# Kernel optimization log

Measured on AMD Instinct MI355X. Metric: run time of the kernel, lower is better.

## Reference

```python
import jax, jax.numpy as jnp
import numpy as np

K = 10
ALPHA = 0.1
N_NODES = 100000
N_EDGES = 3200000
FEATURES = 512
HIDDEN = 256
CLASSES = 64


def setup_inputs() -> dict:
    key = jax.random.key(0)
    k1, k2, k3, k4 = jax.random.split(key, 4)
    x = jax.random.normal(k1, (N_NODES, FEATURES), dtype=jnp.float32)
    edge_index = jax.random.randint(k2, (2, N_EDGES), 0, N_NODES, dtype=jnp.int64)
    W1 = jax.random.normal(k3, (FEATURES, HIDDEN), dtype=jnp.float32) * (1.0 / np.sqrt(FEATURES))
    b1 = jnp.zeros((HIDDEN,), dtype=jnp.float32)
    W2 = jax.random.normal(k4, (HIDDEN, CLASSES), dtype=jnp.float32) * (1.0 / np.sqrt(HIDDEN))
    b2 = jnp.zeros((CLASSES,), dtype=jnp.float32)
    return {"x": x, "edge_index": edge_index, "W1": W1, "b1": b1, "W2": W2, "b2": b2}


def _gcn_norm(edge_index, n_nodes):
    # Add self-loops (APPNP / GCN normalization: D^-1/2 (A+I) D^-1/2)
    loops = jnp.arange(n_nodes, dtype=edge_index.dtype)
    row = jnp.concatenate([edge_index[0], loops])
    col = jnp.concatenate([edge_index[1], loops])
    ones = jnp.ones(row.shape[0], dtype=jnp.float32)
    deg = jax.ops.segment_sum(ones, col, num_segments=n_nodes)
    dinv = jnp.where(deg > 0, jax.lax.rsqrt(deg), 0.0)
    norm = dinv[row] * dinv[col]
    return row, col, norm


def reference(x, edge_index, W1, b1, W2, b2):
    n = x.shape[0]
    h = jax.nn.relu(x @ W1 + b1)          # [N, hidden]
    h = h @ W2 + b2                        # [N, classes]
    row, col, norm = _gcn_norm(edge_index, n)

    def step(out, _):
        msg = out[col] * norm[:, None]     # gather + scale over edges
        agg = jax.ops.segment_sum(msg, row, num_segments=n)
        return (1.0 - ALPHA) * agg + ALPHA * h, None

    out, _ = jax.lax.scan(step, h, None, length=K)
    return jax.nn.log_softmax(out, axis=1)
```

## Files before the change

kernel.cpp:

```cpp
#include <hip/hip_runtime.h>
#include <hip/hip_bf16.h>
#include <math.h>

#define N_NODES 100000
#define N_EDGES 3200000
#define FEAT 512
#define HID 256
#define CLS 64
#define K_ITER 10
#define NBUCK 196
#define BSH 9

typedef _Float16 half8 __attribute__((ext_vector_type(8)));
typedef float f32x4 __attribute__((ext_vector_type(4)));

__device__ __forceinline__ int edge_at(const void* e, int is64, long long idx) {
    return is64 ? (int)((const long long*)e)[idx] : ((const int*)e)[idx];
}

__global__ void k_detect(const unsigned* __restrict__ e, int* __restrict__ flag) {
    __shared__ unsigned s[256];
    unsigned v = 0;
    for (int i = threadIdx.x; i < 4096; i += 256) v |= e[2 * i + 1];
    s[threadIdx.x] = v;
    __syncthreads();
    for (int off = 128; off; off >>= 1) {
        if (threadIdx.x < off) s[threadIdx.x] |= s[threadIdx.x + off];
        __syncthreads();
    }
    if (threadIdx.x == 0) flag[0] = (s[0] == 0) ? 1 : 0;
}

__global__ void k_init(int* __restrict__ bcntR, int* __restrict__ bcntC) {
    for (int i = threadIdx.x; i < NBUCK; i += 256) { bcntR[i] = 0; bcntC[i] = 0; }
}

#define CHB 4096
__global__ __launch_bounds__(256) void k_bhist(const void* __restrict__ e,
                                               const int* __restrict__ flag,
                                               int* __restrict__ bcntR,
                                               int* __restrict__ bcntC) {
    __shared__ int lhR[NBUCK], lhC[NBUCK];
    for (int i = threadIdx.x; i < NBUCK; i += 256) { lhR[i] = 0; lhC[i] = 0; }
    __syncthreads();
    int is64 = flag[0];
    long long base = (long long)blockIdx.x * CHB;
    for (int j = threadIdx.x; j < CHB; j += 256) {
        long long i = base + j;
        if (i < N_EDGES) {
            int r = edge_at(e, is64, i);
            int c = edge_at(e, is64, (long long)N_EDGES + i);
            atomicAdd(&lhR[r >> BSH], 1);
            atomicAdd(&lhC[c >> BSH], 1);
        }
    }
    __syncthreads();
    for (int i = threadIdx.x; i < NBUCK; i += 256) {
        if (lhR[i]) atomicAdd(&bcntR[i], lhR[i]);
        if (lhC[i]) atomicAdd(&bcntC[i], lhC[i]);
    }
}

__global__ void k_bscan(const int* __restrict__ bcntR, const int* __restrict__ bcntC,
                        int* __restrict__ bbaseR, int* __restrict__ gcurR,
                        int* __restrict__ bbaseC, int* __restrict__ gcurC,
                        int* __restrict__ cbase, int* __restrict__ offs) {
    if (threadIdx.x == 0) {
        int accE = 0, accC = 0, accCv = 0;
        for (int b = 0; b < NBUCK; b++) {
            bbaseR[b] = accE;
            gcurR[b] = accE;
            bbaseC[b] = accCv;
            gcurC[b] = accCv;
            cbase[b] = accC;
            int nb0 = b << BSH;
            int nn = (N_NODES - nb0 < 512) ? (N_NODES - nb0) : 512;
            accE += bcntR[b];
            accCv += bcntC[b];
            accC += bcntR[b] + nn;
        }
        bbaseR[NBUCK] = accE;
        bbaseC[NBUCK] = accCv;
        cbase[NBUCK] = accC;
        offs[N_NODES] = accC;
    }
}

#define CH 4096
__global__ __launch_bounds__(256) void k_binA(const void* __restrict__ e,
                                              const int* __restrict__ flag,
                                              int* __restrict__ gcurR,
                                              int* __restrict__ gcurC,
                                              unsigned long long* __restrict__ pairs,
                                              int* __restrict__ cvals) {
    __shared__ int lhR[NBUCK], gbR[NBUCK], lcR[NBUCK];
    __shared__ int lhC[NBUCK], gbC[NBUCK], lcC[NBUCK];
    for (int i = threadIdx.x; i < NBUCK; i += 256) { lhR[i] = 0; lhC[i] = 0; }
    __syncthreads();
    int is64 = flag[0];
    long long base = (long long)blockIdx.x * CH;
    for (int j = threadIdx.x; j < CH; j += 256) {
        long long i = base + j;
        if (i < N_EDGES) {
            int r = edge_at(e, is64, i);
            int c = edge_at(e, is64, (long long)N_EDGES + i);
            atomicAdd(&lhR[r >> BSH], 1);
            atomicAdd(&lhC[c >> BSH], 1);
        }
    }
    __syncthreads();
    for (int i = threadIdx.x; i < NBUCK; i += 256) {
        lcR[i] = 0;
        lcC[i] = 0;
        gbR[i] = lhR[i] ? atomicAdd(&gcurR[i], lhR[i]) : 0;
        gbC[i] = lhC[i] ? atomicAdd(&gcurC[i], lhC[i]) : 0;
    }
    __syncthreads();
    for (int j = threadIdx.x; j < CH; j += 256) {
        long long i = base + j;
        if (i < N_EDGES) {
            int r = edge_at(e, is64, i);
            int c = edge_at(e, is64, (long long)N_EDGES + i);
            int b = r >> BSH;
            int pos = atomicAdd(&lcR[b], 1);
            pairs[(long long)gbR[b] + pos] =
                ((unsigned long long)(unsigned)c << 32) | (unsigned)r;
            int bc = c >> BSH;
            int posc = atomicAdd(&lcC[bc], 1);
            cvals[(long long)gbC[bc] + posc] = c;
        }
    }
}

__global__ __launch_bounds__(1024) void k_degB(const int* __restrict__ cvals,
                                               const int* __restrict__ bbaseC,
                                               float* __restrict__ dinv) {
    __shared__ int cnt[512];
    const int b = blockIdx.x;
    const int nb0 = b << BSH;
    const int nn = (N_NODES - nb0 < 512) ? (N_NODES - nb0) : 512;
    const int t = threadIdx.x;
    if (t < 512) cnt[t] = 1;
    __syncthreads();
    const int e0 = bbaseC[b], e1 = bbaseC[b + 1];
    for (int i = e0 + t; i < e1; i += 1024) {
        atomicAdd(&cnt[cvals[i] - nb0], 1);
    }
    __syncthreads();
    if (t < nn) dinv[nb0 + t] = rsqrtf((float)cnt[t]);
}

__global__ __launch_bounds__(1024) void k_binB(const unsigned long long* __restrict__ pairs,
                                               const int* __restrict__ bbaseR,
                                               const int* __restrict__ cbase,
                                               int* __restrict__ offs,
                                               int* __restrict__ ccol) {
    __shared__ int cnt[512], cur[512], s[512];
    const int b = blockIdx.x;
    const int nb0 = b << BSH;
    const int nn = (N_NODES - nb0 < 512) ? (N_NODES - nb0) : 512;
    const int t = threadIdx.x;
    if (t < 512) cnt[t] = (t < nn) ? 1 : 0;
    __syncthreads();
    const int e0 = bbaseR[b], e1 = bbaseR[b + 1];
    for (int i = e0 + t; i < e1; i += 1024) {
        int r = (int)(pairs[i] & 0xffffffffu);
        atomicAdd(&cnt[r - nb0], 1);
    }
    __syncthreads();
    int v = (t < 512) ? cnt[t] : 0;
    if (t < 512) s[t] = v;
    __syncthreads();
    for (int off = 1; off < 512; off <<= 1) {
        int a = 0;
        if (t < 512 && t >= off) a = s[t - off];
        __syncthreads();
        if (t < 512) s[t] += a;
        __syncthreads();
    }
    const int cb = cbase[b];
    if (t < 512) {
        int excl = s[t] - v;
        cur[t] = excl;
        if (t < nn) {
            offs[nb0 + t] = cb + excl;
            ccol[cb + excl] = nb0 + t;
            cur[t] = excl + 1;
        }
    }
    __syncthreads();
    for (int i = e0 + t; i < e1; i += 1024) {
        unsigned long long p = pairs[i];
        int r = (int)(p & 0xffffffffu);
        int c = (int)(p >> 32);
        int pos = atomicAdd(&cur[r - nb0], 1);
        ccol[cb + pos] = c;
    }
}

__global__ void k_cvtW(const float* __restrict__ W1, const float* __restrict__ W2,
                       _Float16* __restrict__ W1T, _Float16* __restrict__ W2T) {
    int i = blockIdx.x * 256 + threadIdx.x;
    if (i < 256 * 512) {
        int n = i >> 9, k = i & 511;
        W1T[i] = (_Float16)W1[k * 256 + n];
    }
    if (i < 64 * 256) {
        int n = i >> 8, k = i & 255;
        W2T[i] = (_Float16)W2[k * 64 + n];
    }
}

__device__ __forceinline__ int swz(int row, int g) {
    return g ^ (row & 3) ^ ((row >> 2) & 3);
}

__global__ __launch_bounds__(512) void k_gemm1(const float* __restrict__ A,
                                               const _Float16* __restrict__ BT,
                                               const float* __restrict__ bias,
                                               _Float16* __restrict__ C, int M) {
    __shared__ __align__(16) char lds[8192 + 16384];
    const int t = threadIdx.x;
    const int wid = t >> 6, lane = t & 63;
    const int wr = wid >> 2, wc = wid & 3;
    const int srow = t >> 2, sg = t & 3;
    const int fr = lane & 15, fg = lane >> 4;
    const long long by = blockIdx.x;

    f32x4 acc[4][4] = {};
    const long long arow = by * 128 + srow;
    const bool avalid = (arow < M);
    const float* ap0 = A + arow * FEAT + sg * 8;

    for (int kt = 0; kt < FEAT; kt += 32) {
        float4 a0 = make_float4(0.f, 0.f, 0.f, 0.f), a1 = a0;
        if (avalid) {
            const float* ap = ap0 + kt;
            a0 = *(const float4*)ap;
            a1 = *(const float4*)(ap + 4);
        }
        half8 ah;
        ah[0] = (_Float16)a0.x; ah[1] = (_Float16)a0.y;
        ah[2] = (_Float16)a0.z; ah[3] = (_Float16)a0.w;
        ah[4] = (_Float16)a1.x; ah[5] = (_Float16)a1.y;
        ah[6] = (_Float16)a1.z; ah[7] = (_Float16)a1.w;
        *(half8*)(lds + srow * 64 + swz(srow, sg) * 16) = ah;
#pragma unroll
        for (int rep = 0; rep < 2; rep++) {
            int brow = rep * 128 + srow;
            half8 bh = *(const half8*)(BT + brow * FEAT + kt + sg * 8);
            *(half8*)(lds + 8192 + brow * 64 + swz(brow, sg) * 16) = bh;
        }
        __syncthreads();

        half8 af[4], bf[4];
#pragma unroll
        for (int mi = 0; mi < 4; mi++) {
            int r = wr * 64 + mi * 16 + fr;
            af[mi] = *(const half8*)(lds + r * 64 + swz(r, fg) * 16);
        }
#pragma unroll
        for (int nj = 0; nj < 4; nj++) {
            int r = wc * 64 + nj * 16 + fr;
            bf[nj] = *(const half8*)(lds + 8192 + r * 64 + swz(r, fg) * 16);
        }
#pragma unroll
        for (int mi = 0; mi < 4; mi++)
#pragma unroll
            for (int nj = 0; nj < 4; nj++)
                acc[mi][nj] = __builtin_amdgcn_mfma_f32_16x16x32_f16(af[mi], bf[nj], acc[mi][nj], 0, 0, 0);
        __syncthreads();
    }

#pragma unroll
    for (int mi = 0; mi < 4; mi++) {
#pragma unroll
        for (int nj = 0; nj < 4; nj++) {
            int col = wc * 64 + nj * 16 + fr;
            float bv = bias[col];
#pragma unroll
            for (int r = 0; r < 4; r++) {
                long long row = by * 128 + wr * 64 + mi * 16 + fg * 4 + r;
                if (row < M) {
                    float v = fmaxf(acc[mi][nj][r] + bv, 0.f);
                    C[row * HID + col] = (_Float16)v;
                }
            }
        }
    }
}

__global__ __launch_bounds__(512) void k_gemm2(const _Float16* __restrict__ A,
                                               const _Float16* __restrict__ BT,
                                               const float* __restrict__ bias,
                                               const float* __restrict__ dinv,
                                               _Float16* __restrict__ Hout,
                                               _Float16* __restrict__ S0, int M) {
    __shared__ __align__(16) char lds[16384 + 4096];
    const int t = threadIdx.x;
    const int wid = t >> 6, lane = t & 63;
    const int wr = wid >> 1, wc = wid & 1;
    const int srow = t >> 2, sg = t & 3;
    const int fr = lane & 15, fg = lane >> 4;
    const long long bm = blockIdx.x;

    f32x4 acc[4][2] = {};

    for (int kt = 0; kt < HID; kt += 32) {
#pragma unroll
        for (int rep = 0; rep < 2; rep++) {
            int ar = rep * 128 + srow;
            long long grow = bm * 256 + ar;
            if (grow >= M) grow = M - 1;
            half8 ah = *(const half8*)(A + grow * HID + kt + sg * 8);
            *(half8*)(lds + ar * 64 + swz(ar, sg) * 16) = ah;
        }
        if (t < 256) {
            int br = t >> 2;
            half8 bh = *(const half8*)(BT + br * HID + kt + sg * 8);
            *(half8*)(lds + 16384 + br * 64 + swz(br, sg) * 16) = bh;
        }
        __syncthreads();

        half8 af[4], bf[2];
#pragma unroll
        for (int mi = 0; mi < 4; mi++) {
            int r = wr * 64 + mi * 16 + fr;
            af[mi] = *(const half8*)(lds + r * 64 + swz(r, fg) * 16);
        }
#pragma unroll
        for (int nj = 0; nj < 2; nj++) {
            int r = wc * 32 + nj * 16 + fr;
            bf[nj] = *(const half8*)(lds + 16384 + r * 64 + swz(r, fg) * 16);
        }
#pragma unroll
        for (int mi = 0; mi < 4; mi++)
#pragma unroll
            for (int nj = 0; nj < 2; nj++)
                acc[mi][nj] = __builtin_amdgcn_mfma_f32_16x16x32_f16(af[mi], bf[nj], acc[mi][nj], 0, 0, 0);
        __syncthreads();
    }

#pragma unroll
    for (int mi = 0; mi < 4; mi++) {
#pragma unroll
        for (int nj = 0; nj < 2; nj++) {
            int col = wc * 32 + nj * 16 + fr;
            float bv = bias[col];
#pragma unroll
            for (int r = 0; r < 4; r++) {
                long long row = bm * 256 + wr * 64 + mi * 16 + fg * 4 + r;
                if (row < M) {
                    float o = acc[mi][nj][r] + bv;
                    Hout[row * CLS + col] = (_Float16)o;
                    S0[row * CLS + col] = (_Float16)(dinv[row] * o);
                }
            }
        }
    }
}

__global__ __launch_bounds__(256) void k_prop(const int* __restrict__ ccol,
                                              const int* __restrict__ offs,
                                              const float* __restrict__ dinv,
                                              const _Float16* __restrict__ src,
                                              const _Float16* __restrict__ h,
                                              _Float16* __restrict__ dst,
                                              float* __restrict__ out, int last) {
    int wid = (blockIdx.x << 2) + (threadIdx.x >> 6);
    int lane = threadIdx.x & 63;
    if (wid >= N_NODES) return;
    const int g = lane >> 3;
    const int sl = lane & 7;
    const int e0 = offs[wid], e1 = offs[wid + 1];
    float acc[8] = {};
    int e = e0;
    for (; e + 16 <= e1; e += 16) {
        int c0 = ccol[e + g];
        int c1 = ccol[e + 8 + g];
        half8 v0 = *(const half8*)(src + (long long)c0 * CLS + sl * 8);
        half8 v1 = *(const half8*)(src + (long long)c1 * CLS + sl * 8);
#pragma unroll
        for (int j = 0; j < 8; j++) acc[j] += (float)v0[j] + (float)v1[j];
    }
    if (e + 8 <= e1) {
        int c0 = ccol[e + g];
        half8 v0 = *(const half8*)(src + (long long)c0 * CLS + sl * 8);
#pragma unroll
        for (int j = 0; j < 8; j++) acc[j] += (float)v0[j];
        e += 8;
    }
    if (e < e1) {
        int idx = e + g;
        if (idx < e1) {
            int c = ccol[idx];
            half8 v = *(const half8*)(src + (long long)c * CLS + sl * 8);
#pragma unroll
            for (int j = 0; j < 8; j++) acc[j] += (float)v[j];
        }
    }
#pragma unroll
    for (int j = 0; j < 8; j++) {
        acc[j] += __shfl_xor(acc[j], 8);
        acc[j] += __shfl_xor(acc[j], 16);
        acc[j] += __shfl_xor(acc[j], 32);
    }

    float dr = dinv[wid];
    half8 hh = *(const half8*)(h + (long long)wid * CLS + sl * 8);
    float o[8];
#pragma unroll
    for (int j = 0; j < 8; j++) o[j] = 0.9f * dr * acc[j] + 0.1f * (float)hh[j];

    if (!last) {
        if (g == 0) {
            half8 ov;
#pragma unroll
            for (int j = 0; j < 8; j++) ov[j] = (_Float16)(dr * o[j]);
            *(half8*)(dst + (long long)wid * CLS + sl * 8) = ov;
        }
    } else {
        float m = o[0];
#pragma unroll
        for (int j = 1; j < 8; j++) m = fmaxf(m, o[j]);
        m = fmaxf(m, __shfl_xor(m, 1));
        m = fmaxf(m, __shfl_xor(m, 2));
        m = fmaxf(m, __shfl_xor(m, 4));
        float s = 0.f;
#pragma unroll
        for (int j = 0; j < 8; j++) s += expf(o[j] - m);
        s += __shfl_xor(s, 1);
        s += __shfl_xor(s, 2);
        s += __shfl_xor(s, 4);
        float ls = logf(s);
        if (g == 0) {
            float4 ov0 = make_float4(o[0] - m - ls, o[1] - m - ls, o[2] - m - ls, o[3] - m - ls);
            float4 ov1 = make_float4(o[4] - m - ls, o[5] - m - ls, o[6] - m - ls, o[7] - m - ls);
            *(float4*)(out + (long long)wid * CLS + sl * 8) = ov0;
            *(float4*)(out + (long long)wid * CLS + sl * 8 + 4) = ov1;
        }
    }
}

extern "C" void kernel_launch(void* const* d_in, const int* in_sizes, int n_in,
                              void* d_out, int out_size, void* d_ws, size_t ws_size,
                              hipStream_t stream) {
    const float* x  = (const float*)d_in[0];
    const void*  ei = d_in[1];
    const float* W1 = (const float*)d_in[2];
    const float* b1 = (const float*)d_in[3];
    const float* W2 = (const float*)d_in[4];
    const float* b2 = (const float*)d_in[5];
    float* out = (float*)d_out;

    char* p = (char*)d_ws;
    size_t off = 0;
    auto alloc = [&](size_t bytes) {
        char* q = p + off;
        off = (off + bytes + 255) & ~(size_t)255;
        return q;
    };
    int*      flag   = (int*)alloc(16);
    float*    dinv   = (float*)alloc((size_t)N_NODES * 4);
    int*      offs   = (int*)alloc((size_t)(N_NODES + 1) * 4);
    int*      bcntR  = (int*)alloc((NBUCK + 1) * 4);
    int*      bcntC  = (int*)alloc((NBUCK + 1) * 4);
    int*      bbaseR = (int*)alloc((NBUCK + 1) * 4);
    int*      bbaseC = (int*)alloc((NBUCK + 1) * 4);
    int*      cbase  = (int*)alloc((NBUCK + 1) * 4);
    int*      gcurR  = (int*)alloc((NBUCK + 1) * 4);
    int*      gcurC  = (int*)alloc((NBUCK + 1) * 4);
    unsigned long long* pairs = (unsigned long long*)alloc((size_t)N_EDGES * 8);
    int*      cvals  = (int*)alloc((size_t)N_EDGES * 4);
    int*      ccol   = (int*)alloc(((size_t)N_EDGES + N_NODES + 64) * 4);
    _Float16* h      = (_Float16*)alloc((size_t)N_NODES * CLS * 2);
    _Float16* s0     = (_Float16*)alloc((size_t)N_NODES * CLS * 2);
    _Float16* bufA   = (_Float16*)alloc((size_t)N_NODES * CLS * 2);
    _Float16* bufB   = (_Float16*)alloc((size_t)N_NODES * CLS * 2);
    _Float16* h1     = (_Float16*)alloc((size_t)N_NODES * HID * 2);
    _Float16* W1T    = (_Float16*)alloc((size_t)HID * FEAT * 2);
    _Float16* W2T    = (_Float16*)alloc((size_t)CLS * HID * 2);
    (void)ws_size;

    k_detect<<<1, 256, 0, stream>>>((const unsigned*)ei, flag);
    k_init<<<1, 256, 0, stream>>>(bcntR, bcntC);
    k_bhist<<<(N_EDGES + CHB - 1) / CHB, 256, 0, stream>>>(ei, flag, bcntR, bcntC);
    k_bscan<<<1, 64, 0, stream>>>(bcntR, bcntC, bbaseR, gcurR, bbaseC, gcurC, cbase, offs);
    k_binA<<<(N_EDGES + CH - 1) / CH, 256, 0, stream>>>(ei, flag, gcurR, gcurC, pairs, cvals);
    k_degB<<<NBUCK, 1024, 0, stream>>>(cvals, bbaseC, dinv);
    k_binB<<<NBUCK, 1024, 0, stream>>>(pairs, bbaseR, cbase, offs, ccol);

    k_cvtW<<<512, 256, 0, stream>>>(W1, W2, W1T, W2T);
    k_gemm1<<<(N_NODES + 127) / 128, 512, 0, stream>>>(x, W1T, b1, h1, N_NODES);
    k_gemm2<<<(N_NODES + 255) / 256, 512, 0, stream>>>(h1, W2T, b2, dinv, h, s0, N_NODES);

    const int pgrid = (N_NODES + 3) / 4;
    _Float16* ping[2] = {bufA, bufB};
    for (int it = 0; it < K_ITER; it++) {
        const _Float16* src = (it == 0) ? s0 : ping[(it - 1) & 1];
        _Float16* dst = ping[it & 1];
        k_prop<<<pgrid, 256, 0, stream>>>(ccol, offs, dinv, src, h, dst, out, it == K_ITER - 1);
    }
}
```

Before: 824.3 us.

## Pack edge pairs into 32 bits, merge preprocessing kernels, deepen prop unroll

Edge pairs are packed as column<<9 | local row index in 32-bit words instead of 64-bit, which halves the write and read traffic of the binning stage. The degree kernel and the CSR build kernel are merged into one launch with 2*NBUCK blocks, and buffer zeroing is folded into the detect kernel, which removes launches. The propagation loop now gathers 32 edges per step instead of 16, putting more loads in flight. The packing assumes node ids fit in 23 bits, which holds for 100k nodes.

After: 791.5 us. -4.0%, faster.

```diff
diff --git a/kernel.cpp b/kernel.cpp
--- a/kernel.cpp
+++ b/kernel.cpp
@@ -18,7 +18,8 @@
     return is64 ? (int)((const long long*)e)[idx] : ((const int*)e)[idx];
 }
 
-__global__ void k_detect(const unsigned* __restrict__ e, int* __restrict__ flag) {
+__global__ void k_detect(const unsigned* __restrict__ e, int* __restrict__ flag,
+                         int* __restrict__ bcntR, int* __restrict__ bcntC) {
     __shared__ unsigned s[256];
     unsigned v = 0;
     for (int i = threadIdx.x; i < 4096; i += 256) v |= e[2 * i + 1];
@@ -29,10 +30,7 @@
         __syncthreads();
     }
     if (threadIdx.x == 0) flag[0] = (s[0] == 0) ? 1 : 0;
-}
-
-__global__ void k_init(int* __restrict__ bcntR, int* __restrict__ bcntC) {
-    for (int i = threadIdx.x; i < NBUCK; i += 256) { bcntR[i] = 0; bcntC[i] = 0; }
+    if (threadIdx.x < NBUCK) { bcntR[threadIdx.x] = 0; bcntC[threadIdx.x] = 0; }
 }
 
 #define CHB 4096
@@ -91,7 +89,7 @@
                                               const int* __restrict__ flag,
                                               int* __restrict__ gcurR,
                                               int* __restrict__ gcurC,
-                                              unsigned long long* __restrict__ pairs,
+                                              unsigned* __restrict__ pairs,
                                               int* __restrict__ cvals) {
     __shared__ int lhR[NBUCK], gbR[NBUCK], lcR[NBUCK];
     __shared__ int lhC[NBUCK], gbC[NBUCK], lcC[NBUCK];
@@ -123,8 +121,7 @@
             int c = edge_at(e, is64, (long long)N_EDGES + i);
             int b = r >> BSH;
             int pos = atomicAdd(&lcR[b], 1);
-            pairs[(long long)gbR[b] + pos] =
-                ((unsigned long long)(unsigned)c << 32) | (unsigned)r;
+            pairs[(long long)gbR[b] + pos] = ((unsigned)c << 9) | (unsigned)(r & 511);
             int bc = c >> BSH;
             int posc = atomicAdd(&lcC[bc], 1);
             cvals[(long long)gbC[bc] + posc] = c;
@@ -132,40 +129,38 @@
     }
 }
 
-__global__ __launch_bounds__(1024) void k_degB(const int* __restrict__ cvals,
+__global__ __launch_bounds__(1024) void k_bins(const int* __restrict__ cvals,
                                                const int* __restrict__ bbaseC,
-                                               float* __restrict__ dinv) {
-    __shared__ int cnt[512];
-    const int b = blockIdx.x;
-    const int nb0 = b << BSH;
-    const int nn = (N_NODES - nb0 < 512) ? (N_NODES - nb0) : 512;
-    const int t = threadIdx.x;
-    if (t < 512) cnt[t] = 1;
-    __syncthreads();
-    const int e0 = bbaseC[b], e1 = bbaseC[b + 1];
-    for (int i = e0 + t; i < e1; i += 1024) {
-        atomicAdd(&cnt[cvals[i] - nb0], 1);
-    }
-    __syncthreads();
-    if (t < nn) dinv[nb0 + t] = rsqrtf((float)cnt[t]);
-}
-
-__global__ __launch_bounds__(1024) void k_binB(const unsigned long long* __restrict__ pairs,
+                                               float* __restrict__ dinv,
+                                               const unsigned* __restrict__ pairs,
                                                const int* __restrict__ bbaseR,
                                                const int* __restrict__ cbase,
                                                int* __restrict__ offs,
                                                int* __restrict__ ccol) {
     __shared__ int cnt[512], cur[512], s[512];
-    const int b = blockIdx.x;
+    const int t = threadIdx.x;
+    if (blockIdx.x < NBUCK) {
+        const int b = blockIdx.x;
+        const int nb0 = b << BSH;
+        const int nn = (N_NODES - nb0 < 512) ? (N_NODES - nb0) : 512;
+        if (t < 512) cnt[t] = 1;
+        __syncthreads();
+        const int e0 = bbaseC[b], e1 = bbaseC[b + 1];
+        for (int i = e0 + t; i < e1; i += 1024) {
+            atomicAdd(&cnt[cvals[i] - nb0], 1);
+        }
+        __syncthreads();
+        if (t < nn) dinv[nb0 + t] = rsqrtf((float)cnt[t]);
+        return;
+    }
+    const int b = blockIdx.x - NBUCK;
     const int nb0 = b << BSH;
     const int nn = (N_NODES - nb0 < 512) ? (N_NODES - nb0) : 512;
-    const int t = threadIdx.x;
     if (t < 512) cnt[t] = (t < nn) ? 1 : 0;
     __syncthreads();
     const int e0 = bbaseR[b], e1 = bbaseR[b + 1];
     for (int i = e0 + t; i < e1; i += 1024) {
-        int r = (int)(pairs[i] & 0xffffffffu);
-        atomicAdd(&cnt[r - nb0], 1);
+        atomicAdd(&cnt[pairs[i] & 511u], 1);
     }
     __syncthreads();
     int v = (t < 512) ? cnt[t] : 0;
@@ -190,10 +185,10 @@
     }
     __syncthreads();
     for (int i = e0 + t; i < e1; i += 1024) {
-        unsigned long long p = pairs[i];
-        int r = (int)(p & 0xffffffffu);
-        int c = (int)(p >> 32);
-        int pos = atomicAdd(&cur[r - nb0], 1);
+        unsigned p = pairs[i];
+        int r = (int)(p & 511u);
+        int c = (int)(p >> 9);
+        int pos = atomicAdd(&cur[r], 1);
         ccol[cb + pos] = c;
     }
 }
@@ -375,13 +370,27 @@
     const int e0 = offs[wid], e1 = offs[wid + 1];
     float acc[8] = {};
     int e = e0;
-    for (; e + 16 <= e1; e += 16) {
+    for (; e + 32 <= e1; e += 32) {
+        int c0 = ccol[e + g];
+        int c1 = ccol[e + 8 + g];
+        int c2 = ccol[e + 16 + g];
+        int c3 = ccol[e + 24 + g];
+        half8 v0 = *(const half8*)(src + (long long)c0 * CLS + sl * 8);
+        half8 v1 = *(const half8*)(src + (long long)c1 * CLS + sl * 8);
+        half8 v2 = *(const half8*)(src + (long long)c2 * CLS + sl * 8);
+        half8 v3 = *(const half8*)(src + (long long)c3 * CLS + sl * 8);
+#pragma unroll
+        for (int j = 0; j < 8; j++)
+            acc[j] += ((float)v0[j] + (float)v1[j]) + ((float)v2[j] + (float)v3[j]);
+    }
+    if (e + 16 <= e1) {
         int c0 = ccol[e + g];
         int c1 = ccol[e + 8 + g];
         half8 v0 = *(const half8*)(src + (long long)c0 * CLS + sl * 8);
         half8 v1 = *(const half8*)(src + (long long)c1 * CLS + sl * 8);
 #pragma unroll
         for (int j = 0; j < 8; j++) acc[j] += (float)v0[j] + (float)v1[j];
+        e += 16;
     }
     if (e + 8 <= e1) {
         int c0 = ccol[e + g];
@@ -470,7 +479,7 @@
     int*      cbase  = (int*)alloc((NBUCK + 1) * 4);
     int*      gcurR  = (int*)alloc((NBUCK + 1) * 4);
     int*      gcurC  = (int*)alloc((NBUCK + 1) * 4);
-    unsigned long long* pairs = (unsigned long long*)alloc((size_t)N_EDGES * 8);
+    unsigned* pairs  = (unsigned*)alloc((size_t)N_EDGES * 4);
     int*      cvals  = (int*)alloc((size_t)N_EDGES * 4);
     int*      ccol   = (int*)alloc(((size_t)N_EDGES + N_NODES + 64) * 4);
     _Float16* h      = (_Float16*)alloc((size_t)N_NODES * CLS * 2);
@@ -482,13 +491,11 @@
     _Float16* W2T    = (_Float16*)alloc((size_t)CLS * HID * 2);
     (void)ws_size;
 
-    k_detect<<<1, 256, 0, stream>>>((const unsigned*)ei, flag);
-    k_init<<<1, 256, 0, stream>>>(bcntR, bcntC);
+    k_detect<<<1, 256, 0, stream>>>((const unsigned*)ei, flag, bcntR, bcntC);
     k_bhist<<<(N_EDGES + CHB - 1) / CHB, 256, 0, stream>>>(ei, flag, bcntR, bcntC);
     k_bscan<<<1, 64, 0, stream>>>(bcntR, bcntC, bbaseR, gcurR, bbaseC, gcurC, cbase, offs);
     k_binA<<<(N_EDGES + CH - 1) / CH, 256, 0, stream>>>(ei, flag, gcurR, gcurC, pairs, cvals);
-    k_degB<<<NBUCK, 1024, 0, stream>>>(cvals, bbaseC, dinv);
-    k_binB<<<NBUCK, 1024, 0, stream>>>(pairs, bbaseR, cbase, offs, ccol);
+    k_bins<<<2 * NBUCK, 1024, 0, stream>>>(cvals, bbaseC, dinv, pairs, bbaseR, cbase, offs, ccol);
 
     k_cvtW<<<512, 256, 0, stream>>>(W1, W2, W1T, W2T);
     k_gemm1<<<(N_NODES + 127) / 128, 512, 0, stream>>>(x, W1T, b1, h1, N_NODES);
```
